# Kernel tuning notes

Hardware: AMD Instinct MI355X
Metric: run time of the kernel (lower is better)

The kernel has to match this reference:

```python
import jax, jax.numpy as jnp
import numpy as np

D_MODEL = 1024
EXPAND = 2
D_INNER = EXPAND * D_MODEL      # 2048
D_STATE = 2
D_CONV = 4
DT_RANK = (D_MODEL + 15) // 16  # 64
BATCH, SEQ = 2, 4096
LN_EPS = 1e-5


def setup_inputs() -> dict:
    key = jax.random.key(0)
    ks = jax.random.split(key, 16)
    s = 0.02
    inp = {
        "x":       jax.random.normal(ks[0], (BATCH, SEQ, D_MODEL), jnp.float32),
        # Mamba params (torch Linear convention: W is [out, in])
        "w_in":    jax.random.normal(ks[1], (2 * D_INNER, D_MODEL), jnp.float32) * s,
        "conv_w":  jax.random.normal(ks[2], (D_INNER, 1, D_CONV), jnp.float32) * s,
        "conv_b":  jnp.zeros((D_INNER,), jnp.float32),
        "w_xproj": jax.random.normal(ks[3], (DT_RANK + 2 * D_STATE, D_INNER), jnp.float32) * s,
        "w_dt":    jax.random.normal(ks[4], (D_INNER, DT_RANK), jnp.float32) * s,
        "b_dt":    jax.random.normal(ks[5], (D_INNER,), jnp.float32) * s - 4.0,  # softplus -> small dt
        "a_log":   jnp.log(jnp.broadcast_to(jnp.arange(1, D_STATE + 1, dtype=jnp.float32), (D_INNER, D_STATE))),
        "d_skip":  jnp.ones((D_INNER,), jnp.float32),
        "w_out":   jax.random.normal(ks[6], (D_MODEL, D_INNER), jnp.float32) * s,
        # LayerNorms
        "ln1_g":   jnp.ones((D_MODEL,), jnp.float32),
        "ln1_b":   jnp.zeros((D_MODEL,), jnp.float32),
        "ln2_g":   jnp.ones((D_MODEL,), jnp.float32),
        "ln2_b":   jnp.zeros((D_MODEL,), jnp.float32),
        # FFN (Linear d->d, ReLU, Linear d->d; dropout inactive at eval)
        "ffn_w1":  jax.random.normal(ks[7], (D_MODEL, D_MODEL), jnp.float32) * s,
        "ffn_b1":  jnp.zeros((D_MODEL,), jnp.float32),
        "ffn_w2":  jax.random.normal(ks[8], (D_MODEL, D_MODEL), jnp.float32) * s,
        "ffn_b2":  jnp.zeros((D_MODEL,), jnp.float32),
    }
    return inp


def _ln(x, g, b):
    mu = x.mean(-1, keepdims=True)
    v = ((x - mu) ** 2).mean(-1, keepdims=True)
    return (x - mu) * jax.lax.rsqrt(v + LN_EPS) * g + b


def _mamba(x, w_in, conv_w, conv_b, w_xproj, w_dt, b_dt, a_log, d_skip, w_out):
    Bsz = x.shape[0]
    xz = x @ w_in.T                      # (B,L,2*D_INNER)
    xp, z = jnp.split(xz, 2, axis=-1)
    # depthwise causal conv over time
    xc = jnp.transpose(xp, (0, 2, 1))    # (B,D,L)
    xc = jax.lax.conv_general_dilated(
        xc, conv_w, window_strides=(1,), padding=[(D_CONV - 1, 0)],
        feature_group_count=D_INNER)
    xc = xc + conv_b[None, :, None]
    xp = jax.nn.silu(jnp.transpose(xc, (0, 2, 1)))   # (B,L,D)
    # input-dependent SSM params
    x_dbl = xp @ w_xproj.T               # (B,L,DT_RANK+2N)
    dt, Bm, Cm = jnp.split(x_dbl, [DT_RANK, DT_RANK + D_STATE], axis=-1)
    dt = jax.nn.softplus(dt @ w_dt.T + b_dt)          # (B,L,D)
    A = -jnp.exp(a_log)                  # (D,N)
    dA = jnp.exp(dt[..., None] * A)                  # (B,L,D,N)
    dBu = dt[..., None] * Bm[:, :, None, :] * xp[..., None]  # (B,L,D,N)

    def step(h, inp):
        da, dbu, c = inp                 # (B,D,N),(B,D,N),(B,N)
        h = da * h + dbu
        y = jnp.einsum('bdn,bn->bd', h, c)
        return h, y

    h0 = jnp.zeros((Bsz, D_INNER, D_STATE), x.dtype)
    _, ys = jax.lax.scan(step, h0, (jnp.swapaxes(dA, 0, 1),
                                    jnp.swapaxes(dBu, 0, 1),
                                    jnp.swapaxes(Cm, 0, 1)))
    y = jnp.swapaxes(ys, 0, 1)           # (B,L,D)
    y = (y + d_skip * xp) * jax.nn.silu(z)
    return y @ w_out.T                   # (B,L,d_model)


def reference(x, w_in, conv_w, conv_b, w_xproj, w_dt, b_dt, a_log, d_skip, w_out,
              ln1_g, ln1_b, ln2_g, ln2_b, ffn_w1, ffn_b1, ffn_w2, ffn_b2):
    h = x + _mamba(_ln(x, ln1_g, ln1_b), w_in, conv_w, conv_b, w_xproj,
                   w_dt, b_dt, a_log, d_skip, w_out)
    f = _ln(h, ln2_g, ln2_b)
    f = jax.nn.relu(f @ ffn_w1.T + ffn_b1) @ ffn_w2.T + ffn_b2
    return h + f
```

## Files before the change

kernel.cpp:

```cpp
#include <hip/hip_runtime.h>

typedef unsigned short u16;
typedef __bf16 bf16x8 __attribute__((ext_vector_type(8)));
typedef float f32x4 __attribute__((ext_vector_type(4)));
typedef float f32x2 __attribute__((ext_vector_type(2)));
typedef u16 u16x4 __attribute__((ext_vector_type(4)));
typedef u16 u16x8 __attribute__((ext_vector_type(8)));

#define SEQ   4096
#define DM    1024
#define DI    2048
#define NTOK  8192
#define NXP   68
#define DTR   64
#define NCH   4096
#define CHUNK 32
#define NCHK  128

__device__ __forceinline__ float bf2f(u16 v) {
  union { unsigned u; float f; } x; x.u = ((unsigned)v) << 16; return x.f;
}
__device__ __forceinline__ u16 f2bf(float f) {
  unsigned u = __float_as_uint(f);
  return (u16)((u + 0x7FFFu + ((u >> 16) & 1u)) >> 16);
}

__device__ __forceinline__ void g2l16(const u16* g, u16* l) {
  __builtin_amdgcn_global_load_lds(
      (const __attribute__((address_space(1))) unsigned int*)g,
      (__attribute__((address_space(3))) unsigned int*)l, 16, 0, 0);
}

#define SBAR0() __builtin_amdgcn_sched_barrier(0)

__global__ __launch_bounds__(256)
void detect_kernel(const u16* __restrict__ x, int* __restrict__ flag)
{
  __shared__ int tot;
  if (threadIdx.x == 0) tot = 0;
  __syncthreads();
  int cnt = 0;
  for (int i = threadIdx.x; i < 4096; i += 256) {
    const int e = (x[2 * i] >> 7) & 0xFF;
    if (e > 167) cnt++;
  }
  atomicAdd(&tot, cnt);
  __syncthreads();
  if (threadIdx.x == 0) flag[0] = (tot >= 8) ? 1 : 0;
}

#define NW0 4194304
#define NW1  139264
#define NW2  131072
#define NW3 2097152
#define NW4 1048576
#define NW5 1048576
#define NBB 4228
__global__ __launch_bounds__(256)
void convert_all(const float* __restrict__ s0, const float* __restrict__ s1,
                 const float* __restrict__ s2, const float* __restrict__ s3,
                 const float* __restrict__ s4, const float* __restrict__ s5,
                 u16* __restrict__ d0, u16* __restrict__ d1, u16* __restrict__ d2,
                 u16* __restrict__ d3, u16* __restrict__ d4, u16* __restrict__ d5,
                 const void* t0, const void* t1, const void* t2, const void* t3,
                 const void* t4, const void* t5, const void* t6, const void* t7,
                 const void* t8, const void* t9, const void* t10,
                 u16* __restrict__ dsm, const int* __restrict__ flag)
{
  if (blockIdx.x >= NBB) {
    const int i = (blockIdx.x - NBB) * 256 + threadIdx.x;
    if (i >= 24576) return;
    const void* src; int off; int dsti = i;
    if      (i < 8192)  { src = t0;  off = i;
                          dsti = (off & 3) * DI + (off >> 2); }
    else if (i < 10240) { src = t1;  off = i - 8192; }
    else if (i < 12288) { src = t2;  off = i - 10240; }
    else if (i < 16384) { src = t3;  off = i - 12288; }
    else if (i < 18432) { src = t4;  off = i - 16384; }
    else if (i < 19456) { src = t5;  off = i - 18432; }
    else if (i < 20480) { src = t6;  off = i - 19456; }
    else if (i < 21504) { src = t7;  off = i - 20480; }
    else if (i < 22528) { src = t8;  off = i - 21504; }
    else if (i < 23552) { src = t9;  off = i - 22528; }
    else                { src = t10; off = i - 23552; }
    dsm[dsti] = (*flag) ? f2bf(((const float*)src)[off]) : ((const u16*)src)[off];
    return;
  }
  if (*flag == 0) return;
  long e = ((long)blockIdx.x * 256 + threadIdx.x) * 8;
  const long c1 = NW0, c2 = c1 + NW1, c3 = c2 + NW2, c4 = c3 + NW3,
             c5 = c4 + NW4, c6 = c5 + NW5;
  if (e >= c6) return;
  const float* s; u16* d;
  if      (e < c1) { s = s0;          d = d0; }
  else if (e < c2) { s = s1; e -= c1; d = d1; }
  else if (e < c3) { s = s2; e -= c2; d = d2; }
  else if (e < c4) { s = s3; e -= c3; d = d3; }
  else if (e < c5) { s = s4; e -= c4; d = d4; }
  else             { s = s5; e -= c5; d = d5; }
  f32x4 a = *(const f32x4*)(s + e);
  f32x4 b = *(const f32x4*)(s + e + 4);
  u16x8 o;
#pragma unroll
  for (int k = 0; k < 4; ++k) { o[k] = f2bf(a[k]); o[4 + k] = f2bf(b[k]); }
  *(u16x8*)(d + e) = o;
}

template<int MODE>
__global__ __launch_bounds__(256)
void ln_kernel(const void* __restrict__ xin, const u16* __restrict__ gw,
               const u16* __restrict__ bw, u16* __restrict__ outp,
               const int* __restrict__ flag)
{
  const int tid = threadIdx.x;
  const int sub = tid >> 7;
  const int col0 = (tid & 127) * 8;
  const int row = blockIdx.x * 2 + sub;
  const bool isf32 = (MODE == 0) ? (*flag != 0) : false;
  float v[8];
  if (isf32) {
    const float* xf = (const float*)xin + (size_t)row * DM + col0;
    f32x4 a = *(const f32x4*)xf, b2 = *(const f32x4*)(xf + 4);
#pragma unroll
    for (int k = 0; k < 4; ++k) { v[k] = a[k]; v[4 + k] = b2[k]; }
  } else {
    u16x8 xb = *(const u16x8*)((const u16*)xin + (size_t)row * DM + col0);
#pragma unroll
    for (int k = 0; k < 8; ++k) v[k] = bf2f(xb[k]);
  }
  float s = 0.f, s2 = 0.f;
#pragma unroll
  for (int k = 0; k < 8; ++k) { s += v[k]; s2 += v[k] * v[k]; }
#pragma unroll
  for (int off = 32; off > 0; off >>= 1) {
    s  += __shfl_down(s,  off);
    s2 += __shfl_down(s2, off);
  }
  __shared__ float red[4], red2[4];
  __shared__ f32x2 stat[2];
  const int wv = tid >> 6;
  if ((tid & 63) == 0) { red[wv] = s; red2[wv] = s2; }
  __syncthreads();
  if ((tid & 127) == 0) {
    float ts = red[sub * 2] + red[sub * 2 + 1];
    float t2 = red2[sub * 2] + red2[sub * 2 + 1];
    float mu = ts * (1.f / DM);
    float var = t2 * (1.f / DM) - mu * mu;
    stat[sub] = f32x2{mu, rsqrtf(var + 1e-5f)};
  }
  __syncthreads();
  const float mu = stat[sub][0], rs = stat[sub][1];
  u16x8 gv = *(const u16x8*)(gw + col0), bv = *(const u16x8*)(bw + col0);
  u16x8 o;
#pragma unroll
  for (int k = 0; k < 8; ++k)
    o[k] = f2bf((v[k] - mu) * rs * bf2f(gv[k]) + bf2f(bv[k]));
  *(u16x8*)(outp + (size_t)row * DM + col0) = o;
}

template<int EPI, int LNBX>
__global__ __launch_bounds__(512, 2)
void gemm256_kernel(const u16* __restrict__ A, const u16* __restrict__ Bc,
                    const u16* __restrict__ Braw, int M, int N, int K,
                    const int* __restrict__ dtflag, void* __restrict__ Cp,
                    void* __restrict__ Cp2)
{
  __shared__ __align__(16) u16 sAB[2][2][2][128 * 64];
  (void)M;
  const int fl = *dtflag;
  const u16* __restrict__ B = fl ? Bc : Braw;
  const int tid = threadIdx.x;
  const int w = tid >> 6;
  const int lane = tid & 63;
  const int b = blockIdx.x;
  const int wg = (b & 7) * (gridDim.x >> 3) + (b >> 3);
  const int bx = wg & ((1 << LNBX) - 1);
  const int by = wg >> LNBX;
  const int m0 = by * 256;
  const int n0 = bx * 256;
  const int wm = w >> 2;
  const int wn = w & 3;
  const int r = lane & 15;
  const int q = lane >> 4;
  const int r7 = r & 7;
  const int srow = lane >> 3;
  const int schunk = ((lane & 7) ^ (srow & 7)) << 3;

  auto stageA = [&](int buf, int half, int kt) {
#pragma unroll
    for (int j = 0; j < 2; ++j) {
      u16* l = &sAB[buf][0][half][(w * 16 + j * 8) * 64];
      const u16* g = A + (size_t)(m0 + half * 128 + w * 16 + j * 8 + srow) * K
                       + (kt << 6) + schunk;
      g2l16(g, l);
    }
  };
  auto stageB = [&](int buf, int half, int kt) {
#pragma unroll
    for (int j = 0; j < 2; ++j) {
      u16* l = &sAB[buf][1][half][(w * 16 + j * 8) * 64];
      const u16* g = B + (size_t)(n0 + half * 128 + w * 16 + j * 8 + srow) * K
                       + (kt << 6) + schunk;
      g2l16(g, l);
    }
  };

  f32x4 acc[8][4];
#pragma unroll
  for (int i = 0; i < 8; ++i)
#pragma unroll
    for (int j = 0; j < 4; ++j)
#pragma unroll
      for (int t = 0; t < 4; ++t) acc[i][j][t] = 0.f;

  const int nk = K >> 6;
  stageA(0, 0, 0); stageA(0, 1, 0); stageB(0, 0, 0); stageB(0, 1, 0);
  if (nk > 1) { stageB(1, 0, 1); stageB(1, 1, 1); }
  if (nk > 1) asm volatile("s_waitcnt vmcnt(4)" ::: "memory");
  else        asm volatile("s_waitcnt vmcnt(0)" ::: "memory");
  SBAR0();
  __builtin_amdgcn_s_barrier();
  SBAR0();

  for (int kt = 0; kt < nk; ++kt) {
    const int c = kt & 1;
    const u16* bA = &sAB[c][0][wm][0];
    const u16* bB = &sAB[c][1][wn >> 1][0];
    const int rB = (wn & 1) * 64;
    bf16x8 af03[4][2], af47[4][2], b01[2][2], b23[2][2];

#pragma unroll
    for (int mf = 0; mf < 4; ++mf)
#pragma unroll
      for (int ks = 0; ks < 2; ++ks)
        af03[mf][ks] = *(const bf16x8*)&bA[(mf * 16 + r) * 64
                          + ((((ks << 2) + q) ^ r7) << 3)];
#pragma unroll
    for (int nf = 0; nf < 2; ++nf)
#pragma unroll
      for (int ks = 0; ks < 2; ++ks)
        b01[nf][ks] = *(const bf16x8*)&bB[(rB + nf * 16 + r) * 64
                          + ((((ks << 2) + q) ^ r7) << 3)];
    if (kt + 1 < nk) stageA(c ^ 1, 0, kt + 1);
    SBAR0(); __builtin_amdgcn_s_barrier();
    asm volatile("s_waitcnt lgkmcnt(0)" ::: "memory"); SBAR0();
    __builtin_amdgcn_s_setprio(1);
#pragma unroll
    for (int mf = 0; mf < 4; ++mf)
#pragma unroll
      for (int nf = 0; nf < 2; ++nf)
#pragma unroll
        for (int ks = 0; ks < 2; ++ks)
          acc[mf][nf] = __builtin_amdgcn_mfma_f32_16x16x32_bf16(
              af03[mf][ks], b01[nf][ks], acc[mf][nf], 0, 0, 0);
    __builtin_amdgcn_s_setprio(0);
    SBAR0(); __builtin_amdgcn_s_barrier(); SBAR0();

#pragma unroll
    for (int nf = 0; nf < 2; ++nf)
#pragma unroll
      for (int ks = 0; ks < 2; ++ks)
        b23[nf][ks] = *(const bf16x8*)&bB[(rB + (nf + 2) * 16 + r) * 64
                          + ((((ks << 2) + q) ^ r7) << 3)];
    if (kt + 1 < nk) stageA(c ^ 1, 1, kt + 1);
    SBAR0(); __builtin_amdgcn_s_barrier();
    asm volatile("s_waitcnt lgkmcnt(0)" ::: "memory"); SBAR0();
    __builtin_amdgcn_s_setprio(1);
#pragma unroll
    for (int mf = 0; mf < 4; ++mf)
#pragma unroll
      for (int nf = 0; nf < 2; ++nf)
#pragma unroll
        for (int ks = 0; ks < 2; ++ks)
          acc[mf][nf + 2] = __builtin_amdgcn_mfma_f32_16x16x32_bf16(
              af03[mf][ks], b23[nf][ks], acc[mf][nf + 2], 0, 0, 0);
    __builtin_amdgcn_s_setprio(0);
    SBAR0(); __builtin_amdgcn_s_barrier(); SBAR0();

#pragma unroll
    for (int mf = 0; mf < 4; ++mf)
#pragma unroll
      for (int ks = 0; ks < 2; ++ks)
        af47[mf][ks] = *(const bf16x8*)&bA[((mf + 4) * 16 + r) * 64
                          + ((((ks << 2) + q) ^ r7) << 3)];
    if (kt + 2 < nk) stageB(c, 0, kt + 2);
    SBAR0(); __builtin_amdgcn_s_barrier();
    asm volatile("s_waitcnt lgkmcnt(0)" ::: "memory"); SBAR0();
    __builtin_amdgcn_s_setprio(1);
#pragma unroll
    for (int mf = 0; mf < 4; ++mf)
#pragma unroll
      for (int nf = 0; nf < 2; ++nf)
#pragma unroll
        for (int ks = 0; ks < 2; ++ks)
          acc[mf + 4][nf + 2] = __builtin_amdgcn_mfma_f32_16x16x32_bf16(
              af47[mf][ks], b23[nf][ks], acc[mf + 4][nf + 2], 0, 0, 0);
    __builtin_amdgcn_s_setprio(0);
    SBAR0(); __builtin_amdgcn_s_barrier(); SBAR0();

    if (kt + 2 < nk) stageB(c, 1, kt + 2);
    SBAR0(); __builtin_amdgcn_s_barrier(); SBAR0();
    __builtin_amdgcn_s_setprio(1);
#pragma unroll
    for (int mf = 0; mf < 4; ++mf)
#pragma unroll
      for (int nf = 0; nf < 2; ++nf)
#pragma unroll
        for (int ks = 0; ks < 2; ++ks)
          acc[mf + 4][nf] = __builtin_amdgcn_mfma_f32_16x16x32_bf16(
              af47[mf][ks], b01[nf][ks], acc[mf + 4][nf], 0, 0, 0);
    __builtin_amdgcn_s_setprio(0);
    SBAR0();
    if (kt + 2 < nk) asm volatile("s_waitcnt vmcnt(4)" ::: "memory");
    else             asm volatile("s_waitcnt vmcnt(0)" ::: "memory");
    SBAR0();
    __builtin_amdgcn_s_barrier();
    SBAR0();
  }

  float* ep = (float*)&sAB[0][0][0][0] + w * 4096;
  const int r2 = lane >> 2;
  const int ccol = ((lane & 3) ^ (r2 & 3)) * 16;
  u16* C6 = (n0 < DI) ? (u16*)Cp : (u16*)Cp2;
  const int c6off = (n0 < DI) ? 0 : DI;
#pragma unroll
  for (int mf = 0; mf < 8; ++mf) {
#pragma unroll
    for (int nf = 0; nf < 4; ++nf)
#pragma unroll
      for (int t = 0; t < 4; ++t)
        ep[(q * 4 + t) * 68 + nf * 16 + r] = acc[mf][nf][t];
    f32x4 w0 = *(const f32x4*)&ep[r2 * 68 + ccol + 0];
    f32x4 w1 = *(const f32x4*)&ep[r2 * 68 + ccol + 4];
    f32x4 w2 = *(const f32x4*)&ep[r2 * 68 + ccol + 8];
    f32x4 w3 = *(const f32x4*)&ep[r2 * 68 + ccol + 12];
    u16x8 o0, o1;
#pragma unroll
    for (int k = 0; k < 4; ++k) {
      o0[k] = f2bf(w0[k]); o0[4 + k] = f2bf(w1[k]);
      o1[k] = f2bf(w2[k]); o1[4 + k] = f2bf(w3[k]);
    }
    const int row = m0 + wm * 128 + mf * 16 + r2;
    const int colg = n0 + wn * 64 + ccol;
    const size_t cb = (size_t)row * DI + (colg - c6off);
    *(u16x8*)&C6[cb] = o0;
    *(u16x8*)&C6[cb + 8] = o1;
  }
}

template<int EPI, int LNBX>
__global__ __launch_bounds__(256, 2)
void gemm_dp(const u16* __restrict__ A, const u16* __restrict__ Bc,
             const u16* __restrict__ Braw, int M, int N, int K,
             const u16* __restrict__ bias, const u16* __restrict__ addbf,
             const float* __restrict__ addf, const int* __restrict__ dtflag,
             void* __restrict__ Cp, void* __restrict__ Cp2)
{
  __shared__ __align__(16) u16 sA[2][128 * 64];
  __shared__ __align__(16) u16 sB[2][128 * 64];
  (void)M;
  const int fl = *dtflag;
  const u16* __restrict__ B = fl ? Bc : Braw;
  const int tid = threadIdx.x;
  const int lane = tid & 63;
  const int w = tid >> 6;
  const int b = blockIdx.x;
  const int wg = (b & 7) * ((int)gridDim.x >> 3) + (b >> 3);
  const int bx = wg & ((1 << LNBX) - 1);
  const int by = wg >> LNBX;
  const int m0 = by * 128;
  const int n0 = bx * 128;
  const int wm = (w & 1) * 64;
  const int wn = (w >> 1) * 64;
  const int r = lane & 15;
  const int q = lane >> 4;
  const int r7 = lane & 7;
  const int srow = lane >> 3;
  const int schunk = ((lane & 7) ^ (srow & 7)) << 3;

  auto stage = [&](u16* dst, const u16* gbase, int ld) {
#pragma unroll
    for (int j = 0; j < 4; ++j) {
      u16* l = dst + ((j * 4 + w) * 8) * 64;
      const u16* g = gbase + (size_t)((j * 4 + w) * 8 + srow) * ld + schunk;
      g2l16(g, l);
    }
  };
  const u16* gA = A + (size_t)m0 * K;
  const u16* gB = B + (size_t)n0 * K;

  f32x4 acc[4][4];
#pragma unroll
  for (int i = 0; i < 4; ++i)
#pragma unroll
    for (int j = 0; j < 4; ++j)
#pragma unroll
      for (int t = 0; t < 4; ++t) acc[i][j][t] = 0.f;

  const int nk = K >> 6;
  stage(&sA[0][0], gA, K);
  stage(&sB[0][0], gB, K);
  if (nk > 1) {
    stage(&sA[1][0], gA + 64, K);
    asm volatile("s_waitcnt vmcnt(4)" ::: "memory");
  } else {
    asm volatile("s_waitcnt vmcnt(0)" ::: "memory");
  }
  SBAR0();
  __builtin_amdgcn_s_barrier();
  SBAR0();

  for (int kt = 0; kt < nk; ++kt) {
    const int c = kt & 1;
    bf16x8 af[4][2], b01[2][2], b23[2][2];

#pragma unroll
    for (int mf = 0; mf < 4; ++mf)
#pragma unroll
      for (int ks = 0; ks < 2; ++ks)
        af[mf][ks] = *(const bf16x8*)&sA[c][(wm + mf * 16 + r) * 64
                        + ((((ks << 2) + q) ^ r7) << 3)];
#pragma unroll
    for (int nf = 0; nf < 2; ++nf)
#pragma unroll
      for (int ks = 0; ks < 2; ++ks)
        b01[nf][ks] = *(const bf16x8*)&sB[c][(wn + nf * 16 + r) * 64
                        + ((((ks << 2) + q) ^ r7) << 3)];
    if (kt + 1 < nk) stage(&sB[c ^ 1][0], gB + (size_t)(kt + 1) * 64, K);
    SBAR0();
    __builtin_amdgcn_s_barrier();
    SBAR0();
    __builtin_amdgcn_s_setprio(1);
#pragma unroll
    for (int mf = 0; mf < 4; ++mf)
#pragma unroll
      for (int nf = 0; nf < 2; ++nf)
#pragma unroll
        for (int ks = 0; ks < 2; ++ks)
          acc[mf][nf] = __builtin_amdgcn_mfma_f32_16x16x32_bf16(
              af[mf][ks], b01[nf][ks], acc[mf][nf], 0, 0, 0);
    __builtin_amdgcn_s_setprio(0);
    SBAR0();

#pragma unroll
    for (int nf = 0; nf < 2; ++nf)
#pragma unroll
      for (int ks = 0; ks < 2; ++ks)
        b23[nf][ks] = *(const bf16x8*)&sB[c][(wn + (nf + 2) * 16 + r) * 64
                        + ((((ks << 2) + q) ^ r7) << 3)];
    if (kt + 2 < nk) stage(&sA[c][0], gA + (size_t)(kt + 2) * 64, K);
    if (kt + 2 < nk) asm volatile("s_waitcnt vmcnt(4)" ::: "memory");
    else             asm volatile("s_waitcnt vmcnt(0)" ::: "memory");
    SBAR0();
    __builtin_amdgcn_s_barrier();
    SBAR0();
    __builtin_amdgcn_s_setprio(1);
#pragma unroll
    for (int mf = 0; mf < 4; ++mf)
#pragma unroll
      for (int nf = 0; nf < 2; ++nf)
#pragma unroll
        for (int ks = 0; ks < 2; ++ks)
          acc[mf][nf + 2] = __builtin_amdgcn_mfma_f32_16x16x32_bf16(
              af[mf][ks], b23[nf][ks], acc[mf][nf + 2], 0, 0, 0);
    __builtin_amdgcn_s_setprio(0);
    SBAR0();
  }

  __syncthreads();
  float* ep = (w < 2) ? ((float*)&sA[0][0] + w * 2048)
                      : ((float*)&sB[0][0] + (w - 2) * 2048);
  const int r2 = lane >> 2;
  const int ccol = ((lane & 3) ^ (r2 & 3)) * 16;
#pragma unroll
  for (int i = 0; i < 4; ++i) {
#pragma unroll
    for (int j = 0; j < 4; ++j)
#pragma unroll
      for (int t = 0; t < 4; ++t)
        ep[(q * 4 + t) * 68 + j * 16 + r] = acc[i][j][t];
    f32x4 w0 = *(const f32x4*)&ep[r2 * 68 + ccol + 0];
    f32x4 w1 = *(const f32x4*)&ep[r2 * 68 + ccol + 4];
    f32x4 w2 = *(const f32x4*)&ep[r2 * 68 + ccol + 8];
    f32x4 w3 = *(const f32x4*)&ep[r2 * 68 + ccol + 12];
    float vv[16];
#pragma unroll
    for (int k = 0; k < 4; ++k) {
      vv[k] = w0[k]; vv[4 + k] = w1[k]; vv[8 + k] = w2[k]; vv[12 + k] = w3[k];
    }
    const int row = m0 + wm + i * 16 + r2;
    const int colg = n0 + wn + ccol;
    const size_t idx = (size_t)row * N + colg;
    if (EPI == 3) {
      float ax[16];
      if (fl) {
        f32x4 a0 = *(const f32x4*)&addf[idx];
        f32x4 a1 = *(const f32x4*)&addf[idx + 4];
        f32x4 a2 = *(const f32x4*)&addf[idx + 8];
        f32x4 a3 = *(const f32x4*)&addf[idx + 12];
#pragma unroll
        for (int k = 0; k < 4; ++k) {
          ax[k] = a0[k]; ax[4 + k] = a1[k]; ax[8 + k] = a2[k]; ax[12 + k] = a3[k];
        }
      } else {
        u16x8 a0 = *(const u16x8*)&addbf[idx];
        u16x8 a1 = *(const u16x8*)&addbf[idx + 8];
#pragma unroll
        for (int k = 0; k < 8; ++k) { ax[k] = bf2f(a0[k]); ax[8 + k] = bf2f(a1[k]); }
      }
      u16x8 o0, o1;
#pragma unroll
      for (int k = 0; k < 8; ++k) {
        o0[k] = f2bf(vv[k] + ax[k]); o1[k] = f2bf(vv[8 + k] + ax[8 + k]);
      }
      *(u16x8*)&((u16*)Cp)[idx] = o0;
      *(u16x8*)&((u16*)Cp)[idx + 8] = o1;
    } else if (EPI == 4) {
      u16x8 b0 = *(const u16x8*)&bias[colg];
      u16x8 b1 = *(const u16x8*)&bias[colg + 8];
      u16x8 o0, o1;
#pragma unroll
      for (int k = 0; k < 8; ++k) {
        o0[k] = f2bf(fmaxf(vv[k] + bf2f(b0[k]), 0.f));
        o1[k] = f2bf(fmaxf(vv[8 + k] + bf2f(b1[k]), 0.f));
      }
      *(u16x8*)&((u16*)Cp)[idx] = o0;
      *(u16x8*)&((u16*)Cp)[idx + 8] = o1;
    } else {
      u16x8 b0 = *(const u16x8*)&bias[colg];
      u16x8 b1 = *(const u16x8*)&bias[colg + 8];
      u16x8 a0 = *(const u16x8*)&addbf[idx];
      u16x8 a1 = *(const u16x8*)&addbf[idx + 8];
      float r0[8], r1[8];
#pragma unroll
      for (int k = 0; k < 8; ++k) {
        r0[k] = vv[k] + bf2f(b0[k]) + bf2f(a0[k]);
        r1[k] = vv[8 + k] + bf2f(b1[k]) + bf2f(a1[k]);
      }
      if (fl) {
        f32x4 f0, f1, f2, f3;
#pragma unroll
        for (int k = 0; k < 4; ++k) { f0[k] = r0[k]; f1[k] = r0[4 + k]; f2[k] = r1[k]; f3[k] = r1[4 + k]; }
        *(f32x4*)&((float*)Cp)[idx] = f0;
        *(f32x4*)&((float*)Cp)[idx + 4] = f1;
        *(f32x4*)&((float*)Cp)[idx + 8] = f2;
        *(f32x4*)&((float*)Cp)[idx + 12] = f3;
      } else {
        u16x8 o0, o1;
#pragma unroll
        for (int k = 0; k < 8; ++k) { o0[k] = f2bf(r0[k]); o1[k] = f2bf(r1[k]); }
        *(u16x8*)&((u16*)Cp)[idx] = o0;
        *(u16x8*)&((u16*)Cp)[idx + 8] = o1;
      }
    }
  }
}

template<int LNBX>
__global__ __launch_bounds__(256, 2)
void gemm_k64(const u16* __restrict__ A, const u16* __restrict__ Bc,
              const u16* __restrict__ Braw, const int* __restrict__ dtflag,
              const u16* __restrict__ bias, u16* __restrict__ Cp)
{
  __shared__ __align__(16) u16 sA[128 * 64];
  __shared__ __align__(16) u16 sB[128 * 64];
  const int fl = *dtflag;
  const u16* __restrict__ B = fl ? Bc : Braw;
  const int tid = threadIdx.x;
  const int lane = tid & 63;
  const int w = tid >> 6;
  const int b = blockIdx.x;
  const int wg = (b & 7) * ((int)gridDim.x >> 3) + (b >> 3);
  const int bx = wg & ((1 << LNBX) - 1);
  const int by = wg >> LNBX;
  const int m0 = by * 128;
  const int n0 = bx * 128;
  const int wm = (w & 1) * 64;
  const int wn = (w >> 1) * 64;
  const int r = lane & 15;
  const int q = lane >> 4;
  const int r7 = lane & 7;
  const int srow = lane >> 3;
  const int schunk = ((lane & 7) ^ (srow & 7)) << 3;

  auto stage = [&](u16* dst, const u16* gbase) {
#pragma unroll
    for (int j = 0; j < 4; ++j) {
      u16* l = dst + ((j * 4 + w) * 8) * 64;
      const u16* g = gbase + (size_t)((j * 4 + w) * 8 + srow) * 64 + schunk;
      g2l16(g, l);
    }
  };
  stage(&sA[0], A + (size_t)m0 * 64);
  stage(&sB[0], B + (size_t)n0 * 64);
  asm volatile("s_waitcnt vmcnt(0)" ::: "memory");
  SBAR0();
  __builtin_amdgcn_s_barrier();
  SBAR0();

  f32x4 acc[4][4];
#pragma unroll
  for (int i = 0; i < 4; ++i)
#pragma unroll
    for (int j = 0; j < 4; ++j)
#pragma unroll
      for (int t = 0; t < 4; ++t) acc[i][j][t] = 0.f;

  bf16x8 af[4][2], bfv[4][2];
#pragma unroll
  for (int mf = 0; mf < 4; ++mf)
#pragma unroll
    for (int ks = 0; ks < 2; ++ks)
      af[mf][ks] = *(const bf16x8*)&sA[(wm + mf * 16 + r) * 64
                      + ((((ks << 2) + q) ^ r7) << 3)];
#pragma unroll
  for (int nf = 0; nf < 4; ++nf)
#pragma unroll
    for (int ks = 0; ks < 2; ++ks)
      bfv[nf][ks] = *(const bf16x8*)&sB[(wn + nf * 16 + r) * 64
                      + ((((ks << 2) + q) ^ r7) << 3)];
#pragma unroll
  for (int mf = 0; mf < 4; ++mf)
#pragma unroll
    for (int nf = 0; nf < 4; ++nf)
#pragma unroll
      for (int ks = 0; ks < 2; ++ks)
        acc[mf][nf] = __builtin_amdgcn_mfma_f32_16x16x32_bf16(
            af[mf][ks], bfv[nf][ks], acc[mf][nf], 0, 0, 0);

  __syncthreads();
  float* ep = (w < 2) ? ((float*)&sA[0] + w * 2048)
                      : ((float*)&sB[0] + (w - 2) * 2048);
  const int r2 = lane >> 2;
  const int ccol = ((lane & 3) ^ (r2 & 3)) * 16;
#pragma unroll
  for (int i = 0; i < 4; ++i) {
#pragma unroll
    for (int j = 0; j < 4; ++j)
#pragma unroll
      for (int t = 0; t < 4; ++t)
        ep[(q * 4 + t) * 68 + j * 16 + r] = acc[i][j][t];
    f32x4 w0 = *(const f32x4*)&ep[r2 * 68 + ccol + 0];
    f32x4 w1 = *(const f32x4*)&ep[r2 * 68 + ccol + 4];
    f32x4 w2 = *(const f32x4*)&ep[r2 * 68 + ccol + 8];
    f32x4 w3 = *(const f32x4*)&ep[r2 * 68 + ccol + 12];
    float vv[16];
#pragma unroll
    for (int k = 0; k < 4; ++k) {
      vv[k] = w0[k]; vv[4 + k] = w1[k]; vv[8 + k] = w2[k]; vv[12 + k] = w3[k];
    }
    const int row = m0 + wm + i * 16 + r2;
    const int colg = n0 + wn + ccol;
    const size_t idx = (size_t)row * DI + colg;
    u16x8 b0 = *(const u16x8*)&bias[colg];
    u16x8 b1 = *(const u16x8*)&bias[colg + 8];
    u16x8 o0, o1;
#pragma unroll
    for (int k = 0; k < 8; ++k) {
      float v0 = vv[k] + bf2f(b0[k]);
      float v1 = vv[8 + k] + bf2f(b1[k]);
      v0 = (v0 > 15.f) ? v0 : __logf(1.f + __expf(v0));
      v1 = (v1 > 15.f) ? v1 : __logf(1.f + __expf(v1));
      o0[k] = f2bf(v0); o1[k] = f2bf(v1);
    }
    *(u16x8*)&Cp[idx] = o0;
    *(u16x8*)&Cp[idx + 8] = o1;
  }
}

__global__ __launch_bounds__(256, 2)
void xproj_splitk(const u16* __restrict__ A, const u16* __restrict__ Bc,
                  const u16* __restrict__ Braw, const int* __restrict__ dtflag,
                  float* __restrict__ part)
{
  __shared__ __align__(16) u16 sA[2][128 * 32];
  __shared__ __align__(16) u16 sB[2][128 * 32];
  const int fl = *dtflag;
  const u16* __restrict__ B = fl ? Bc : Braw;
  const int tid = threadIdx.x;
  const int kz = blockIdx.x;
  const int m0 = blockIdx.y * 128;
  const int kbase = kz * 256;
  const int lane = tid & 63;
  const int wv = tid >> 6;
  const int wm = (wv & 1) * 64;
  const int wn = (wv >> 1) * 64;
  const int r = lane & 15;
  const int q = lane >> 4;
  const int rsw = (r >> 1) & 3;
  const int pr = lane >> 2;
  const int kc = (lane & 3) ^ ((pr >> 1) & 3);
  const int pk = kc * 8;

  u16* lA0[2] = { &sA[0][(wv * 2 + 0) * 512], &sA[1][(wv * 2 + 0) * 512] };
  u16* lA1[2] = { &sA[0][(wv * 2 + 1) * 512], &sA[1][(wv * 2 + 1) * 512] };
  u16* lB0[2] = { &sB[0][(wv * 2 + 0) * 512], &sB[1][(wv * 2 + 0) * 512] };
  u16* lB1[2] = { &sB[0][(wv * 2 + 1) * 512], &sB[1][(wv * 2 + 1) * 512] };
  int br0 = wv * 32 + pr;      if (br0 > 67) br0 = 67;
  int br1 = wv * 32 + 16 + pr; if (br1 > 67) br1 = 67;
  const u16* gA0 = A + (size_t)(m0 + wv * 32 + pr) * DI + kbase + pk;
  const u16* gA1 = gA0 + (size_t)16 * DI;
  const u16* gB0 = B + (size_t)br0 * DI + kbase + pk;
  const u16* gB1 = B + (size_t)br1 * DI + kbase + pk;

  f32x4 acc[4][4];
#pragma unroll
  for (int i = 0; i < 4; ++i)
#pragma unroll
    for (int j = 0; j < 4; ++j)
#pragma unroll
      for (int t = 0; t < 4; ++t) acc[i][j][t] = 0.f;

  g2l16(gA0, lA0[0]); g2l16(gA1, lA1[0]);
  g2l16(gB0, lB0[0]); g2l16(gB1, lB1[0]);

  for (int kt = 0; kt < 8; ++kt) {
    const int cur = kt & 1;
    __syncthreads();
    bf16x8 af[4], bfr[4];
#pragma unroll
    for (int i = 0; i < 4; ++i)
      af[i] = *reinterpret_cast<const bf16x8*>(
          &sA[cur][(wm + i * 16 + r) * 32 + (q ^ rsw) * 8]);
#pragma unroll
    for (int j = 0; j < 4; ++j)
      bfr[j] = *reinterpret_cast<const bf16x8*>(
          &sB[cur][(wn + j * 16 + r) * 32 + (q ^ rsw) * 8]);
    if (kt + 1 < 8) {
      gA0 += 32; gA1 += 32; gB0 += 32; gB1 += 32;
      g2l16(gA0, lA0[cur ^ 1]); g2l16(gA1, lA1[cur ^ 1]);
      g2l16(gB0, lB0[cur ^ 1]); g2l16(gB1, lB1[cur ^ 1]);
    }
#pragma unroll
    for (int i = 0; i < 4; ++i)
#pragma unroll
      for (int j = 0; j < 4; ++j)
        acc[i][j] = __builtin_amdgcn_mfma_f32_16x16x32_bf16(af[i], bfr[j], acc[i][j], 0, 0, 0);
  }

#pragma unroll
  for (int i = 0; i < 4; ++i)
#pragma unroll
    for (int j = 0; j < 4; ++j)
#pragma unroll
      for (int t = 0; t < 4; ++t) {
        const int row = m0 + wm + i * 16 + q * 4 + t;
        const int col = wn + j * 16 + r;
        if (col < NXP)
          part[((size_t)kz * NTOK + row) * NXP + col] = acc[i][j][t];
      }
}

__global__ __launch_bounds__(256)
void xreduce_kernel(const float* __restrict__ part, u16* __restrict__ dtraw,
                    float* __restrict__ bc)
{
  const int i = blockIdx.x * 256 + threadIdx.x;
  if (i >= NTOK * NXP) return;
  const int row = i / NXP, col = i - row * NXP;
  float s = 0.f;
#pragma unroll
  for (int z = 0; z < 8; ++z) s += part[(size_t)z * NTOK * NXP + i];
  if (col < DTR) dtraw[(size_t)row * DTR + col] = f2bf(s);
  else           bc[row * 4 + (col - DTR)] = s;
}

#define CTT 16
__global__ __launch_bounds__(256)
void conv_silu_tok(const u16* __restrict__ xp, const u16* __restrict__ cwT,
                   const u16* __restrict__ cb, u16* __restrict__ u)
{
  const int tok0 = blockIdx.x * CTT;
  const int t0 = tok0 & (SEQ - 1);
  const int d0 = threadIdx.x * 8;
  float w[4][8], cbv[8];
#pragma unroll
  for (int j = 0; j < 4; ++j) {
    u16x8 wv = *(const u16x8*)(cwT + j * DI + d0);
#pragma unroll
    for (int k = 0; k < 8; ++k) w[j][k] = bf2f(wv[k]);
  }
  u16x8 cbb = *(const u16x8*)(cb + d0);
#pragma unroll
  for (int k = 0; k < 8; ++k) cbv[k] = bf2f(cbb[k]);
  float xm0[8], xm1[8], xm2[8];
#pragma unroll
  for (int k = 0; k < 8; ++k) { xm0[k] = 0.f; xm1[k] = 0.f; xm2[k] = 0.f; }
  if (t0 != 0) {
    u16x8 a = *(const u16x8*)(xp + (size_t)(tok0 - 3) * DI + d0);
    u16x8 bb = *(const u16x8*)(xp + (size_t)(tok0 - 2) * DI + d0);
    u16x8 c = *(const u16x8*)(xp + (size_t)(tok0 - 1) * DI + d0);
#pragma unroll
    for (int k = 0; k < 8; ++k) {
      xm0[k] = bf2f(a[k]); xm1[k] = bf2f(bb[k]); xm2[k] = bf2f(c[k]);
    }
  }
#pragma unroll
  for (int i = 0; i < CTT; ++i) {
    u16x8 xv = *(const u16x8*)(xp + (size_t)(tok0 + i) * DI + d0);
    float xc[8];
    u16x8 o;
#pragma unroll
    for (int k = 0; k < 8; ++k) {
      xc[k] = bf2f(xv[k]);
      const float a = cbv[k] + w[0][k] * xm0[k] + w[1][k] * xm1[k]
                    + w[2][k] * xm2[k] + w[3][k] * xc[k];
      const float sg = 1.f / (1.f + __expf(-a));
      o[k] = f2bf(a * sg);
    }
    *(u16x8*)(u + (size_t)(tok0 + i) * DI + d0) = o;
#pragma unroll
    for (int k = 0; k < 8; ++k) { xm0[k] = xm1[k]; xm1[k] = xm2[k]; xm2[k] = xc[k]; }
  }
}

__global__ __launch_bounds__(256)
void scan_pass1(const u16* __restrict__ dtb, const u16* __restrict__ ub,
                const float* __restrict__ bc, const u16* __restrict__ a_log,
                float* __restrict__ S, float* __restrict__ hf0, float* __restrict__ hf1)
{
  const int g4 = blockIdx.x * 256 + threadIdx.x;
  const int chg = g4 & (NCH / 4 - 1);
  const int c = g4 >> 10;
  const int ch0 = chg * 4;
  const int b = ch0 >> 11;
  const int d0 = ch0 & (DI - 1);
  u16x8 av = *(const u16x8*)(a_log + d0 * 2);
  float A0[4], A1[4];
#pragma unroll
  for (int k = 0; k < 4; ++k) {
    A0[k] = -__expf(bf2f(av[2 * k]));
    A1[k] = -__expf(bf2f(av[2 * k + 1]));
  }
  float h0[4] = {0.f, 0.f, 0.f, 0.f}, h1[4] = {0.f, 0.f, 0.f, 0.f};
  float s[4] = {0.f, 0.f, 0.f, 0.f};
  const int row0 = b * SEQ + c * CHUNK;
  for (int i = 0; i < CHUNK; ++i) {
    const size_t row = row0 + i;
    u16x4 dtv = *(const u16x4*)(dtb + row * DI + d0);
    u16x4 uv  = *(const u16x4*)(ub + row * DI + d0);
    f32x2 Bv = *(const f32x2*)(bc + row * 4);
#pragma unroll
    for (int k = 0; k < 4; ++k) {
      const float dt = bf2f(dtv[k]);
      const float dtu = dt * bf2f(uv[k]);
      h0[k] = __expf(A0[k] * dt) * h0[k] + dtu * Bv[0];
      h1[k] = __expf(A1[k] * dt) * h1[k] + dtu * Bv[1];
      s[k] += dt;
    }
  }
  const size_t g0 = (size_t)c * NCH + ch0;
  *(f32x4*)(S + g0)   = f32x4{s[0], s[1], s[2], s[3]};
  *(f32x4*)(hf0 + g0) = f32x4{h0[0], h0[1], h0[2], h0[3]};
  *(f32x4*)(hf1 + g0) = f32x4{h1[0], h1[1], h1[2], h1[3]};
}

__global__ __launch_bounds__(256)
void scan_pass2(const float* __restrict__ S, const float* __restrict__ hf0,
                const float* __restrict__ hf1, const u16* __restrict__ a_log,
                float* __restrict__ hi0, float* __restrict__ hi1)
{
  const int ch = blockIdx.x * 256 + threadIdx.x;
  const int d = ch & (DI - 1);
  const float A0 = -__expf(bf2f(a_log[d * 2 + 0]));
  const float A1 = -__expf(bf2f(a_log[d * 2 + 1]));
  float h0 = 0.f, h1 = 0.f;
  size_t g = ch;
  float sv = S[g], f0 = hf0[g], f1 = hf1[g];
  for (int c = 0; c < NCHK; ++c) {
    float svn = 0.f, f0n = 0.f, f1n = 0.f;
    if (c + 1 < NCHK) {
      const size_t gn = g + NCH;
      svn = S[gn]; f0n = hf0[gn]; f1n = hf1[gn];
    }
    hi0[g] = h0; hi1[g] = h1;
    h0 = __expf(A0 * sv) * h0 + f0;
    h1 = __expf(A1 * sv) * h1 + f1;
    sv = svn; f0 = f0n; f1 = f1n;
    g += NCH;
  }
}

__global__ __launch_bounds__(256)
void scan_pass3(const u16* __restrict__ dtb, const u16* __restrict__ ub,
                const float* __restrict__ bc, const u16* __restrict__ zbuf,
                const u16* __restrict__ a_log, const u16* __restrict__ d_skip,
                const float* __restrict__ hi0, const float* __restrict__ hi1,
                u16* __restrict__ yb)
{
  const int g4 = blockIdx.x * 256 + threadIdx.x;
  const int chg = g4 & (NCH / 4 - 1);
  const int c = g4 >> 10;
  const int ch0 = chg * 4;
  const int b = ch0 >> 11;
  const int d0 = ch0 & (DI - 1);
  u16x8 av = *(const u16x8*)(a_log + d0 * 2);
  u16x4 dkv = *(const u16x4*)(d_skip + d0);
  float A0[4], A1[4], dsk[4];
#pragma unroll
  for (int k = 0; k < 4; ++k) {
    A0[k] = -__expf(bf2f(av[2 * k]));
    A1[k] = -__expf(bf2f(av[2 * k + 1]));
    dsk[k] = bf2f(dkv[k]);
  }
  const size_t g0 = (size_t)c * NCH + ch0;
  f32x4 h0v = *(const f32x4*)(hi0 + g0);
  f32x4 h1v = *(const f32x4*)(hi1 + g0);
  float h0[4], h1[4];
#pragma unroll
  for (int k = 0; k < 4; ++k) { h0[k] = h0v[k]; h1[k] = h1v[k]; }
  const int row0 = b * SEQ + c * CHUNK;
  for (int i = 0; i < CHUNK; ++i) {
    const size_t row = row0 + i;
    u16x4 dtv = *(const u16x4*)(dtb + row * DI + d0);
    u16x4 uv  = *(const u16x4*)(ub + row * DI + d0);
    u16x4 zv  = *(const u16x4*)(zbuf + row * DI + d0);
    f32x4 bcv = *(const f32x4*)(bc + row * 4);
    u16x4 o;
#pragma unroll
    for (int k = 0; k < 4; ++k) {
      const float dt = bf2f(dtv[k]);
      const float uu = bf2f(uv[k]);
      const float dtu = dt * uu;
      h0[k] = __expf(A0[k] * dt) * h0[k] + dtu * bcv[0];
      h1[k] = __expf(A1[k] * dt) * h1[k] + dtu * bcv[1];
      const float y = h0[k] * bcv[2] + h1[k] * bcv[3];
      const float z = bf2f(zv[k]);
      const float sz = z / (1.f + __expf(-z));
      o[k] = f2bf((y + dsk[k] * uu) * sz);
    }
    *(u16x4*)(yb + row * DI + d0) = o;
  }
}

extern "C" void kernel_launch(void* const* d_in, const int* in_sizes, int n_in,
                              void* d_out, int out_size, void* d_ws, size_t ws_size,
                              hipStream_t stream)
{
  const void* x       = d_in[0];
  const void* w_in    = d_in[1];
  const void* conv_w  = d_in[2];
  const void* conv_b  = d_in[3];
  const void* w_xproj = d_in[4];
  const void* w_dt    = d_in[5];
  const void* b_dt    = d_in[6];
  const void* a_log   = d_in[7];
  const void* d_skip  = d_in[8];
  const void* w_out   = d_in[9];
  const void* ln1_g   = d_in[10];
  const void* ln1_b   = d_in[11];
  const void* ln2_g   = d_in[12];
  const void* ln2_b   = d_in[13];
  const void* ffn_w1  = d_in[14];
  const void* ffn_b1  = d_in[15];
  const void* ffn_w2  = d_in[16];
  const void* ffn_b2  = d_in[17];
  char* ws = (char*)d_ws;

  const size_t o_flag  = 0;
  const size_t o_small = 256;
  const size_t o_cwout = o_small + 65536;
  const size_t o_cff1  = o_cwout + (size_t)DM * DI * 2;
  const size_t o_cff2  = o_cff1  + (size_t)DM * DM * 2;
  const size_t o_cxp   = o_cff2  + (size_t)DM * DM * 2;
  const size_t o_cwdt  = o_cxp   + (size_t)NXP * DI * 2;
  const size_t o_xn    = 9437184;
  const size_t o_xp    = o_xn + (size_t)NTOK * DM * 2;
  const size_t o_z     = o_xp + (size_t)NTOK * DI * 2;
  const size_t o_u     = o_z  + (size_t)NTOK * DI * 2;
  const size_t o_bc    = o_u  + (size_t)NTOK * DI * 2;
  const size_t SCN = (size_t)NCHK * NCH * 4;
  const size_t o_S   = o_xn + 0 * SCN;
  const size_t o_hf0 = o_xn + 1 * SCN;
  const size_t o_hf1 = o_xn + 2 * SCN;
  const size_t o_hi0 = o_xn + 3 * SCN;
  const size_t o_hi1 = o_xn + 4 * SCN;

  int*   flagp   = (int*)(ws + o_flag);
  u16*   csmall  = (u16*)(ws + o_small);
  u16*   c_cwT   = csmall +     0;
  u16*   c_convb = csmall +  8192;
  u16*   c_bdt   = csmall + 10240;
  u16*   c_alog  = csmall + 12288;
  u16*   c_dskip = csmall + 16384;
  u16*   c_ln1g  = csmall + 18432;
  u16*   c_ln1b  = csmall + 19456;
  u16*   c_ln2g  = csmall + 20480;
  u16*   c_ln2b  = csmall + 21504;
  u16*   c_fb1   = csmall + 22528;
  u16*   c_fb2   = csmall + 23552;
  u16*   c_wout  = (u16*)(ws + o_cwout);
  u16*   c_ff1   = (u16*)(ws + o_cff1);
  u16*   c_ff2   = (u16*)(ws + o_cff2);
  u16*   c_xproj = (u16*)(ws + o_cxp);
  u16*   c_wdt   = (u16*)(ws + o_cwdt);
  u16*   c_win   = (u16*)(ws + o_u);
  u16*   xn      = (u16*)(ws + o_xn);
  u16*   xp      = (u16*)(ws + o_xp);
  u16*   zb      = (u16*)(ws + o_z);
  u16*   u       = (u16*)(ws + o_u);
  float* part    = (float*)(ws + o_xp);
  u16*   dtraw   = (u16*)(ws + o_xn);
  u16*   dtb     = xp;
  u16*   yb      = xp;
  float* bc      = (float*)(ws + o_bc);
  float* S       = (float*)(ws + o_S);
  float* hf0     = (float*)(ws + o_hf0);
  float* hf1     = (float*)(ws + o_hf1);
  float* hi0     = (float*)(ws + o_hi0);
  float* hi1     = (float*)(ws + o_hi1);
  u16*   hb      = (u16*)(ws + o_z);
  u16*   hn      = (u16*)(ws + o_xn);
  u16*   f1      = (u16*)(ws + o_u);

  const dim3 blk(256);

  detect_kernel<<<1, blk, 0, stream>>>((const u16*)x, flagp);
  convert_all<<<NBB + 96, blk, 0, stream>>>(
      (const float*)w_in, (const float*)w_xproj, (const float*)w_dt,
      (const float*)w_out, (const float*)ffn_w1, (const float*)ffn_w2,
      c_win, c_xproj, c_wdt, c_wout, c_ff1, c_ff2,
      conv_w, conv_b, b_dt, a_log, d_skip,
      ln1_g, ln1_b, ln2_g, ln2_b, ffn_b1, ffn_b2,
      csmall, flagp);

  ln_kernel<0><<<NTOK / 2, blk, 0, stream>>>(x, c_ln1g, c_ln1b, xn, flagp);
  gemm256_kernel<6, 4><<<512, dim3(512), 0, stream>>>(
      xn, c_win, (const u16*)w_in, NTOK, 2 * DI, DM, flagp, xp, zb);
  conv_silu_tok<<<NTOK / CTT, blk, 0, stream>>>(xp, c_cwT, c_convb, u);
  xproj_splitk<<<dim3(8, 64), blk, 0, stream>>>(u, c_xproj, (const u16*)w_xproj,
                                                flagp, part);
  xreduce_kernel<<<(NTOK * NXP + 255) / 256, blk, 0, stream>>>(part, dtraw, bc);
  gemm_k64<4><<<1024, blk, 0, stream>>>(dtraw, c_wdt, (const u16*)w_dt,
                                        flagp, c_bdt, dtb);
  scan_pass1<<<NCHK * NCH / 4 / 256, blk, 0, stream>>>(dtb, u, bc, c_alog, S, hf0, hf1);
  scan_pass2<<<NCH / 256, blk, 0, stream>>>(S, hf0, hf1, c_alog, hi0, hi1);
  scan_pass3<<<NCHK * NCH / 4 / 256, blk, 0, stream>>>(dtb, u, bc, zb, c_alog, c_dskip,
                                                       hi0, hi1, yb);
  gemm_dp<3, 3><<<512, blk, 0, stream>>>(yb, c_wout, (const u16*)w_out,
                                         NTOK, DM, DI,
                                         nullptr, (const u16*)x, (const float*)x,
                                         flagp, hb, nullptr);
  ln_kernel<1><<<NTOK / 2, blk, 0, stream>>>(hb, c_ln2g, c_ln2b, hn, flagp);
  gemm_dp<4, 3><<<512, blk, 0, stream>>>(hn, c_ff1, (const u16*)ffn_w1,
                                         NTOK, DM, DM,
                                         c_fb1, nullptr, nullptr, flagp, f1, nullptr);
  gemm_dp<5, 3><<<512, blk, 0, stream>>>(f1, c_ff2, (const u16*)ffn_w2,
                                         NTOK, DM, DM,
                                         c_fb2, hb, nullptr, flagp, d_out, nullptr);
}
```

Measured before the change: 438.6 us.

## Merge four-phase GEMM mainloop into two phases with fewer barriers

Restructures the in_proj GEMM main loop from four barrier-separated MFMA phases into two. Each phase now loads more LDS fragments (b01 and b23 together) and issues both stage calls back to back. This cuts the per-iteration workgroup barriers from about five to two, reducing synchronization stalls, at the cost of higher register pressure and coarser interleaving of memory and compute. The staging of B for kt+2 into buffer c now happens after a single barrier placed once the af47 reads are done.

```diff
diff --git a/kernel.cpp b/kernel.cpp
--- a/kernel.cpp
+++ b/kernel.cpp
@@ -238,11 +238,13 @@
 #pragma unroll
     for (int nf = 0; nf < 2; ++nf)
 #pragma unroll
-      for (int ks = 0; ks < 2; ++ks)
+      for (int ks = 0; ks < 2; ++ks) {
         b01[nf][ks] = *(const bf16x8*)&bB[(rB + nf * 16 + r) * 64
                           + ((((ks << 2) + q) ^ r7) << 3)];
-    if (kt + 1 < nk) stageA(c ^ 1, 0, kt + 1);
-    SBAR0(); __builtin_amdgcn_s_barrier();
+        b23[nf][ks] = *(const bf16x8*)&bB[(rB + (nf + 2) * 16 + r) * 64
+                          + ((((ks << 2) + q) ^ r7) << 3)];
+      }
+    if (kt + 1 < nk) { stageA(c ^ 1, 0, kt + 1); stageA(c ^ 1, 1, kt + 1); }
     asm volatile("s_waitcnt lgkmcnt(0)" ::: "memory"); SBAR0();
     __builtin_amdgcn_s_setprio(1);
 #pragma unroll
@@ -250,32 +252,14 @@
 #pragma unroll
       for (int nf = 0; nf < 2; ++nf)
 #pragma unroll
-        for (int ks = 0; ks < 2; ++ks)
+        for (int ks = 0; ks < 2; ++ks) {
           acc[mf][nf] = __builtin_amdgcn_mfma_f32_16x16x32_bf16(
               af03[mf][ks], b01[nf][ks], acc[mf][nf], 0, 0, 0);
-    __builtin_amdgcn_s_setprio(0);
-    SBAR0(); __builtin_amdgcn_s_barrier(); SBAR0();
-
-#pragma unroll
-    for (int nf = 0; nf < 2; ++nf)
-#pragma unroll
-      for (int ks = 0; ks < 2; ++ks)
-        b23[nf][ks] = *(const bf16x8*)&bB[(rB + (nf + 2) * 16 + r) * 64
-                          + ((((ks << 2) + q) ^ r7) << 3)];
-    if (kt + 1 < nk) stageA(c ^ 1, 1, kt + 1);
-    SBAR0(); __builtin_amdgcn_s_barrier();
-    asm volatile("s_waitcnt lgkmcnt(0)" ::: "memory"); SBAR0();
-    __builtin_amdgcn_s_setprio(1);
-#pragma unroll
-    for (int mf = 0; mf < 4; ++mf)
-#pragma unroll
-      for (int nf = 0; nf < 2; ++nf)
-#pragma unroll
-        for (int ks = 0; ks < 2; ++ks)
           acc[mf][nf + 2] = __builtin_amdgcn_mfma_f32_16x16x32_bf16(
               af03[mf][ks], b23[nf][ks], acc[mf][nf + 2], 0, 0, 0);
+        }
     __builtin_amdgcn_s_setprio(0);
-    SBAR0(); __builtin_amdgcn_s_barrier(); SBAR0();
+    SBAR0();
 
 #pragma unroll
     for (int mf = 0; mf < 4; ++mf)
@@ -283,8 +267,10 @@
       for (int ks = 0; ks < 2; ++ks)
         af47[mf][ks] = *(const bf16x8*)&bA[((mf + 4) * 16 + r) * 64
                           + ((((ks << 2) + q) ^ r7) << 3)];
-    if (kt + 2 < nk) stageB(c, 0, kt + 2);
-    SBAR0(); __builtin_amdgcn_s_barrier();
+    SBAR0();
+    __builtin_amdgcn_s_barrier();
+    SBAR0();
+    if (kt + 2 < nk) { stageB(c, 0, kt + 2); stageB(c, 1, kt + 2); }
     asm volatile("s_waitcnt lgkmcnt(0)" ::: "memory"); SBAR0();
     __builtin_amdgcn_s_setprio(1);
 #pragma unroll
@@ -292,23 +278,12 @@
 #pragma unroll
       for (int nf = 0; nf < 2; ++nf)
 #pragma unroll
-        for (int ks = 0; ks < 2; ++ks)
+        for (int ks = 0; ks < 2; ++ks) {
+          acc[mf + 4][nf] = __builtin_amdgcn_mfma_f32_16x16x32_bf16(
+              af47[mf][ks], b01[nf][ks], acc[mf + 4][nf], 0, 0, 0);
           acc[mf + 4][nf + 2] = __builtin_amdgcn_mfma_f32_16x16x32_bf16(
               af47[mf][ks], b23[nf][ks], acc[mf + 4][nf + 2], 0, 0, 0);
-    __builtin_amdgcn_s_setprio(0);
-    SBAR0(); __builtin_amdgcn_s_barrier(); SBAR0();
-
-    if (kt + 2 < nk) stageB(c, 1, kt + 2);
-    SBAR0(); __builtin_amdgcn_s_barrier(); SBAR0();
-    __builtin_amdgcn_s_setprio(1);
-#pragma unroll
-    for (int mf = 0; mf < 4; ++mf)
-#pragma unroll
-      for (int nf = 0; nf < 2; ++nf)
-#pragma unroll
-        for (int ks = 0; ks < 2; ++ks)
-          acc[mf + 4][nf] = __builtin_amdgcn_mfma_f32_16x16x32_bf16(
-              af47[mf][ks], b01[nf][ks], acc[mf + 4][nf], 0, 0, 0);
+        }
     __builtin_amdgcn_s_setprio(0);
     SBAR0();
     if (kt + 2 < nk) asm volatile("s_waitcnt vmcnt(4)" ::: "memory");
```

New measurement: 433.3 us. No clear change (-1.2%).
